# Kernel optimization log

Hardware: AMD Instinct MI355X
Metric: run time of the kernel (lower is better)

## Reference

```python
import jax, jax.numpy as jnp
import numpy as np


def setup_inputs() -> dict:
    key = jax.random.key(0)
    k1, k2, k3, k4, k5 = jax.random.split(key, 5)
    in_f, out_f, rank = 4096, 4096, 16
    std = 1.0 / np.sqrt(rank)
    x = jax.random.normal(k1, (4, 2048, in_f), dtype=jnp.float32)
    base_weight = jax.random.normal(k2, (out_f, in_f), dtype=jnp.float32) * 0.02
    lora_A = jax.random.normal(k3, (rank, in_f), dtype=jnp.float32) * std
    lora_B = jax.random.normal(k4, (out_f, rank), dtype=jnp.float32) * 0.01
    magnitude_vec = jax.random.uniform(k5, (out_f,), dtype=jnp.float32) + 0.5
    return {"x": x, "base_weight": base_weight, "lora_A": lora_A,
            "lora_B": lora_B, "magnitude_vec": magnitude_vec}


def reference(x, base_weight, lora_A, lora_B, magnitude_vec):
    # x: [B, S, in] -> tokens [N, in]
    out_shape = (*x.shape[:-1], base_weight.shape[0])
    xt = x.reshape(-1, x.shape[-1])
    # low-rank adapter path: [N, rank] @ [rank, out]
    lora_out = (xt @ lora_A.T) @ lora_B.T
    # column-wise L2 norm of adapted weight, per output row: [out]
    adapted_w = base_weight + lora_B @ lora_A
    column_norm = jnp.linalg.norm(adapted_w, axis=1)
    magnitude_scale = magnitude_vec / column_norm  # [out]
    # base GEMM + adapter + magnitude rescale epilogue
    dora_out = (xt @ base_weight.T + lora_out) * magnitude_scale[None, :]
    return dora_out.reshape(out_shape)
```

## Files before the change

kernel.cpp:

```cpp
#include <hip/hip_runtime.h>
#include <hip/hip_bf16.h>
#include <stdint.h>

typedef __attribute__((ext_vector_type(8))) short s16x8;
typedef __attribute__((ext_vector_type(4))) float f32x4;
typedef __attribute__((ext_vector_type(4))) unsigned short us4;

__device__ inline unsigned short bf_rne(float f) {
    union { float f; uint32_t u; } v; v.f = f;
    uint32_t u = v.u;
    u += 0x7FFFu + ((u >> 16) & 1u);
    return (unsigned short)(u >> 16);
}

#define GLD_LDS16(gp, lp)                                                     \
    __builtin_amdgcn_global_load_lds(                                         \
        (const __attribute__((address_space(1))) void*)(gp),                  \
        (__attribute__((address_space(3))) void*)(lp), 16, 0, 0)

#define LDSOFF(p) ((unsigned)(uintptr_t)(__attribute__((address_space(3))) const void*)(p))

__global__ __launch_bounds__(256) void prologue_kernel(
    const float4* __restrict__ x4, us4* __restrict__ xbf4,
    const float4* __restrict__ W4,
    const float4* __restrict__ A4,
    const float* __restrict__ B,
    const float* __restrict__ mag,
    unsigned short* __restrict__ wbf,
    float* __restrict__ scale) {
    const int tid = threadIdx.x;
    if (blockIdx.x < 512) {
        const int m0 = blockIdx.x * 8;
        __shared__ float Bs[8][16];
        __shared__ float red[32];
        if (tid < 128) Bs[tid >> 4][tid & 15] = B[m0 * 16 + tid];
        __syncthreads();
        float ss[8] = {};
        for (int c = tid; c < 1024; c += 256) {
            float4 a[16];
#pragma unroll
            for (int r = 0; r < 16; ++r) a[r] = A4[r * 1024 + c];
#pragma unroll
            for (int i = 0; i < 8; ++i) {
                float4 w = W4[(size_t)(m0 + i) * 1024 + c];
#pragma unroll
                for (int r = 0; r < 16; ++r) {
                    const float br = Bs[i][r];
                    w.x += br * a[r].x; w.y += br * a[r].y;
                    w.z += br * a[r].z; w.w += br * a[r].w;
                }
                ss[i] += w.x * w.x + w.y * w.y + w.z * w.z + w.w * w.w;
                us4 o; o[0] = bf_rne(w.x); o[1] = bf_rne(w.y);
                o[2] = bf_rne(w.z); o[3] = bf_rne(w.w);
                *(us4*)&wbf[(size_t)(m0 + i) * 4096 + c * 4] = o;
            }
        }
        const int lane = tid & 63, wv = tid >> 6;
#pragma unroll
        for (int i = 0; i < 8; ++i) {
            float v = ss[i];
#pragma unroll
            for (int off = 32; off > 0; off >>= 1) v += __shfl_down(v, off, 64);
            if (lane == 0) red[wv * 8 + i] = v;
        }
        __syncthreads();
        if (tid < 8) {
            float tot = red[tid] + red[8 + tid] + red[16 + tid] + red[24 + tid];
            scale[m0 + tid] = mag[m0 + tid] / sqrtf(tot);
        }
    } else {
        const size_t base = (size_t)(blockIdx.x - 512) * 1024 + tid;
#pragma unroll
        for (int j = 0; j < 4; ++j) {
            const size_t idx = base + j * 256;
            float4 a = x4[idx];
            us4 o;
            o[0] = bf_rne(a.x); o[1] = bf_rne(a.y);
            o[2] = bf_rne(a.z); o[3] = bf_rne(a.w);
            xbf4[idx] = o;
        }
    }
}

#define FENCE() asm volatile("" ::: "memory")
#define BAR()   do { FENCE(); __builtin_amdgcn_s_barrier(); FENCE(); } while (0)
#define VMW6()  asm volatile("s_waitcnt vmcnt(6)" ::: "memory")
#define VMW0()  asm volatile("s_waitcnt vmcnt(0)" ::: "memory")
#define LGW(n)  asm volatile("s_waitcnt lgkmcnt(" #n ")" ::: "memory")
#define SB0()   __builtin_amdgcn_sched_barrier(0)
#define PRIO1() __builtin_amdgcn_s_setprio(1)
#define PRIO0() __builtin_amdgcn_s_setprio(0)

#define DSR(dst, va, IMM) \
    asm volatile("ds_read_b128 %0, %1 offset:" #IMM : "=v"(dst) : "v"(va))

__global__ __launch_bounds__(512, 2) void dora_gemm(
    const unsigned short* __restrict__ xbf,
    const unsigned short* __restrict__ wbf,
    const float* __restrict__ scale,
    float* __restrict__ out) {
    __shared__ __align__(16) unsigned short As[2][256 * 64];
    __shared__ __align__(16) unsigned short Bs[2][256 * 64];

    const int tid  = threadIdx.x;
    const int lane = tid & 63;
    const int w    = tid >> 6;
    const int wm   = w >> 2;
    const int wn   = w & 3;
    const int q    = lane >> 4;
    const int c15  = lane & 15;

    const int bid = blockIdx.x;
    const int xcd = bid & 7, sub = bid >> 3;
    const int tileM = (((xcd & 3) << 3) | (sub & 7)) << 8;
    const int tileN = (((xcd >> 2) << 3) | (sub >> 3)) << 8;

    const int r0 = tid >> 3;
    const int lc = (tid & 7) ^ (r0 & 7);
    const size_t aoff = (size_t)(tileM + r0) * 4096 + lc * 8;
    const size_t boff = (size_t)(tileN + r0) * 4096 + lc * 8;
    const int ld0 = (w * 64) * 8;
    const int ld1 = (512 + w * 64) * 8;

#define STAGE_A(d, h, k0) do {                                                            \
    GLD_LDS16(xbf + aoff + (size_t)((h) * 128) * 4096 + (k0),      &As[d][(h) * 8192 + ld0]); \
    GLD_LDS16(xbf + aoff + (size_t)((h) * 128 + 64) * 4096 + (k0), &As[d][(h) * 8192 + ld1]); \
} while (0)
#define STAGE_B(d, h, k0) do {                                                            \
    GLD_LDS16(wbf + boff + (size_t)((h) * 128) * 4096 + (k0),      &Bs[d][(h) * 8192 + ld0]); \
    GLD_LDS16(wbf + boff + (size_t)((h) * 128 + 64) * 4096 + (k0), &Bs[d][(h) * 8192 + ld1]); \
} while (0)

    const int rb = c15 & 7;
    unsigned aA[4][2], aB[2][2];
#pragma unroll
    for (int mt = 0; mt < 4; ++mt)
#pragma unroll
        for (int kc = 0; kc < 2; ++kc)
            aA[mt][kc] = LDSOFF(&As[0][(wm * 64 + mt * 16 + c15) * 64 +
                                       ((kc * 4 + q) ^ rb) * 8]);
#pragma unroll
    for (int nt = 0; nt < 2; ++nt)
#pragma unroll
        for (int kc = 0; kc < 2; ++kc)
            aB[nt][kc] = LDSOFF(&Bs[0][(wn * 32 + nt * 16 + c15) * 64 +
                                       ((kc * 4 + q) ^ rb) * 8]);

    s16x8 af[4][2];
    s16x8 bfx[2][2][2];
    f32x4 acc[8][4] = {};

#define RD16(I0, I1) do {                                                     \
    DSR(bfx[0][0][0], aB[0][0], I0); DSR(bfx[0][1][0], aB[1][0], I0);         \
    DSR(af[0][0], aA[0][0], I0);     DSR(af[1][0], aA[1][0], I0);             \
    DSR(af[2][0], aA[2][0], I0);     DSR(af[3][0], aA[3][0], I0);             \
    DSR(bfx[0][0][1], aB[0][1], I0); DSR(bfx[0][1][1], aB[1][1], I0);         \
    DSR(af[0][1], aA[0][1], I0);     DSR(af[1][1], aA[1][1], I0);             \
    DSR(af[2][1], aA[2][1], I0);     DSR(af[3][1], aA[3][1], I0);             \
    DSR(bfx[1][0][0], aB[0][0], I1); DSR(bfx[1][1][0], aB[1][0], I1);         \
    DSR(bfx[1][0][1], aB[0][1], I1); DSR(bfx[1][1][1], aB[1][1], I1); } while (0)
#define RD_A1(IMM) do {                                                       \
    DSR(af[0][0], aA[0][0], IMM); DSR(af[1][0], aA[1][0], IMM);               \
    DSR(af[2][0], aA[2][0], IMM); DSR(af[3][0], aA[3][0], IMM);               \
    DSR(af[0][1], aA[0][1], IMM); DSR(af[1][1], aA[1][1], IMM);               \
    DSR(af[2][1], aA[2][1], IMM); DSR(af[3][1], aA[3][1], IMM); } while (0)

#define MFMA_H(mh, nh, kcv) do {                                              \
    _Pragma("unroll") for (int mt = 0; mt < 4; ++mt)                          \
    _Pragma("unroll") for (int nt = 0; nt < 2; ++nt)                          \
        acc[(mh) * 4 + mt][(nh) * 2 + nt] =                                   \
            __builtin_amdgcn_mfma_f32_16x16x32_bf16(                          \
                af[mt][kcv], bfx[nh][nt][kcv],                                \
                acc[(mh) * 4 + mt][(nh) * 2 + nt], 0, 0, 0);                  \
} while (0)
#define MFMA_Q(mh, nh) do { MFMA_H(mh, nh, 0); MFMA_H(mh, nh, 1); } while (0)

    STAGE_A(0, 0, 0); STAGE_B(0, 0, 0); STAGE_B(0, 1, 0); STAGE_A(0, 1, 0);
    STAGE_A(1, 0, 64); STAGE_B(1, 0, 64); STAGE_B(1, 1, 64);
    VMW6(); BAR();

    for (int t0k = 0; t0k <= 60 * 64; t0k += 128) {
        const int kt1 = t0k + 64;
        const int kn2 = t0k + 128;
        const int kn3 = t0k + 192;
        RD16(0, 16384);
        STAGE_A(1, 1, kt1);
        BAR();
        LGW(10); SB0(); PRIO1(); MFMA_H(0, 0, 0); PRIO0();
        LGW(4);  SB0(); PRIO1(); MFMA_H(0, 0, 1); PRIO0();
        BAR();
        LGW(0); SB0(); PRIO1(); MFMA_Q(0, 1); PRIO0();
        RD_A1(16384);
        STAGE_A(0, 0, kn2); STAGE_B(0, 0, kn2);
        BAR();
        LGW(4); SB0(); PRIO1(); MFMA_H(1, 1, 0); PRIO0();
        LGW(0); SB0(); PRIO1(); MFMA_H(1, 1, 1); PRIO0();
        STAGE_B(0, 1, kn2);
        VMW6(); BAR();
        PRIO1(); MFMA_Q(1, 0); PRIO0();
        RD16(32768, 49152);
        STAGE_A(0, 1, kn2);
        BAR();
        LGW(10); SB0(); PRIO1(); MFMA_H(0, 0, 0); PRIO0();
        LGW(4);  SB0(); PRIO1(); MFMA_H(0, 0, 1); PRIO0();
        BAR();
        LGW(0); SB0(); PRIO1(); MFMA_Q(0, 1); PRIO0();
        RD_A1(49152);
        STAGE_A(1, 0, kn3); STAGE_B(1, 0, kn3);
        BAR();
        LGW(4); SB0(); PRIO1(); MFMA_H(1, 1, 0); PRIO0();
        LGW(0); SB0(); PRIO1(); MFMA_H(1, 1, 1); PRIO0();
        STAGE_B(1, 1, kn3);
        VMW6(); BAR();
        PRIO1(); MFMA_Q(1, 0); PRIO0();
    }

    RD16(0, 16384);
    STAGE_A(1, 1, 4032);
    BAR();
    LGW(10); SB0(); PRIO1(); MFMA_H(0, 0, 0); PRIO0();
    LGW(4);  SB0(); PRIO1(); MFMA_H(0, 0, 1); PRIO0();
    BAR();
    LGW(0); SB0(); PRIO1(); MFMA_Q(0, 1); PRIO0();
    RD_A1(16384);
    BAR();
    LGW(4); SB0(); PRIO1(); MFMA_H(1, 1, 0); PRIO0();
    LGW(0); SB0(); PRIO1(); MFMA_H(1, 1, 1); PRIO0();
    VMW0(); BAR();
    PRIO1(); MFMA_Q(1, 0); PRIO0();
    RD16(32768, 49152);
    LGW(10); SB0(); PRIO1(); MFMA_H(0, 0, 0); PRIO0();
    LGW(4);  SB0(); PRIO1(); MFMA_H(0, 0, 1); PRIO0();
    LGW(0);  SB0(); PRIO1(); MFMA_Q(0, 1); PRIO0();
    RD_A1(49152);
    LGW(4); SB0(); PRIO1(); MFMA_H(1, 1, 0); PRIO0();
    LGW(0); SB0(); PRIO1(); MFMA_H(1, 1, 1); MFMA_Q(1, 0); PRIO0();

#pragma unroll
    for (int nh = 0; nh < 2; ++nh)
#pragma unroll
    for (int nt = 0; nt < 2; ++nt) {
        const int col = tileN + nh * 128 + wn * 32 + nt * 16 + c15;
        const float s = scale[col];
#pragma unroll
        for (int mh = 0; mh < 2; ++mh)
#pragma unroll
        for (int mt = 0; mt < 4; ++mt) {
            const int row0 = tileM + mh * 128 + wm * 64 + mt * 16 + q * 4;
#pragma unroll
            for (int r = 0; r < 4; ++r)
                out[(size_t)(row0 + r) * 4096 + col] = acc[mh * 4 + mt][nh * 2 + nt][r] * s;
        }
    }
}

extern "C" void kernel_launch(void* const* d_in, const int* in_sizes, int n_in,
                              void* d_out, int out_size, void* d_ws, size_t ws_size,
                              hipStream_t stream) {
    const float* x   = (const float*)d_in[0];
    const float* W   = (const float*)d_in[1];
    const float* A   = (const float*)d_in[2];
    const float* B   = (const float*)d_in[3];
    const float* mag = (const float*)d_in[4];
    float* out = (float*)d_out;

    const size_t XBF_BYTES = (size_t)8192 * 4096 * 2;
    const size_t WBF_BYTES = (size_t)4096 * 4096 * 2;
    const size_t NEEDED = XBF_BYTES + WBF_BYTES + 4096 * sizeof(float);
    if (ws_size < NEEDED) return;

    unsigned short* xbf = (unsigned short*)d_ws;
    unsigned short* wbf = (unsigned short*)((char*)d_ws + XBF_BYTES);
    float* scale = (float*)((char*)d_ws + XBF_BYTES + WBF_BYTES);

    prologue_kernel<<<8704, 256, 0, stream>>>((const float4*)x, (us4*)xbf,
                                              (const float4*)W, (const float4*)A,
                                              B, mag, wbf, scale);
    dora_gemm<<<512, 512, 0, stream>>>(xbf, wbf, scale, out);
}
```

Baseline: 307.2 us.

## Load B operand directly from global into registers, dropping LDS staging for weights

The weight (B) tile is no longer staged through shared memory. Each wave now issues buffer_load_dwordx4 straight into its MFMA operand registers, and only the activation tile goes through LDS. The main loop is rewritten into a simpler two-tile pipeline with fewer barriers. This halves LDS footprint and LDS read traffic, but B data is no longer shared across the waves in a block, so global/L2 traffic for weights grows and load latency must be hidden by the register prefetch.

```diff
diff --git a/kernel.cpp b/kernel.cpp
--- a/kernel.cpp
+++ b/kernel.cpp
@@ -5,6 +5,7 @@
 typedef __attribute__((ext_vector_type(8))) short s16x8;
 typedef __attribute__((ext_vector_type(4))) float f32x4;
 typedef __attribute__((ext_vector_type(4))) unsigned short us4;
+typedef __attribute__((ext_vector_type(4))) unsigned int u32x4;
 
 __device__ inline unsigned short bf_rne(float f) {
     union { float f; uint32_t u; } v; v.f = f;
@@ -84,8 +85,7 @@
 
 #define FENCE() asm volatile("" ::: "memory")
 #define BAR()   do { FENCE(); __builtin_amdgcn_s_barrier(); FENCE(); } while (0)
-#define VMW6()  asm volatile("s_waitcnt vmcnt(6)" ::: "memory")
-#define VMW0()  asm volatile("s_waitcnt vmcnt(0)" ::: "memory")
+#define VMW(n)  asm volatile("s_waitcnt vmcnt(" #n ")" ::: "memory")
 #define LGW(n)  asm volatile("s_waitcnt lgkmcnt(" #n ")" ::: "memory")
 #define SB0()   __builtin_amdgcn_sched_barrier(0)
 #define PRIO1() __builtin_amdgcn_s_setprio(1)
@@ -93,6 +93,10 @@
 
 #define DSR(dst, va, IMM) \
     asm volatile("ds_read_b128 %0, %1 offset:" #IMM : "=v"(dst) : "v"(va))
+
+#define BLD(dst, voff) \
+    asm volatile("buffer_load_dwordx4 %0, %1, %2, 0 offen" \
+                 : "=v"(dst) : "v"(voff), "s"(srd))
 
 __global__ __launch_bounds__(512, 2) void dora_gemm(
     const unsigned short* __restrict__ xbf,
@@ -100,7 +104,6 @@
     const float* __restrict__ scale,
     float* __restrict__ out) {
     __shared__ __align__(16) unsigned short As[2][256 * 64];
-    __shared__ __align__(16) unsigned short Bs[2][256 * 64];
 
     const int tid  = threadIdx.x;
     const int lane = tid & 63;
@@ -118,7 +121,6 @@
     const int r0 = tid >> 3;
     const int lc = (tid & 7) ^ (r0 & 7);
     const size_t aoff = (size_t)(tileM + r0) * 4096 + lc * 8;
-    const size_t boff = (size_t)(tileN + r0) * 4096 + lc * 8;
     const int ld0 = (w * 64) * 8;
     const int ld1 = (512 + w * 64) * 8;
 
@@ -126,44 +128,45 @@
     GLD_LDS16(xbf + aoff + (size_t)((h) * 128) * 4096 + (k0),      &As[d][(h) * 8192 + ld0]); \
     GLD_LDS16(xbf + aoff + (size_t)((h) * 128 + 64) * 4096 + (k0), &As[d][(h) * 8192 + ld1]); \
 } while (0)
-#define STAGE_B(d, h, k0) do {                                                            \
-    GLD_LDS16(wbf + boff + (size_t)((h) * 128) * 4096 + (k0),      &Bs[d][(h) * 8192 + ld0]); \
-    GLD_LDS16(wbf + boff + (size_t)((h) * 128 + 64) * 4096 + (k0), &Bs[d][(h) * 8192 + ld1]); \
-} while (0)
 
     const int rb = c15 & 7;
-    unsigned aA[4][2], aB[2][2];
+    unsigned aA[4][2];
 #pragma unroll
     for (int mt = 0; mt < 4; ++mt)
 #pragma unroll
         for (int kc = 0; kc < 2; ++kc)
             aA[mt][kc] = LDSOFF(&As[0][(wm * 64 + mt * 16 + c15) * 64 +
                                        ((kc * 4 + q) ^ rb) * 8]);
-#pragma unroll
-    for (int nt = 0; nt < 2; ++nt)
-#pragma unroll
-        for (int kc = 0; kc < 2; ++kc)
-            aB[nt][kc] = LDSOFF(&Bs[0][(wn * 32 + nt * 16 + c15) * 64 +
-                                       ((kc * 4 + q) ^ rb) * 8]);
+
+    const unsigned long long wb = (unsigned long long)(uintptr_t)wbf;
+    const u32x4 srd = { (unsigned)wb, (unsigned)(wb >> 32),
+                        0xFFFFFFFFu, 0x00020000u };
+    unsigned v000 = (unsigned)((tileN + wn * 32 + c15) * 8192 + q * 16);
+    unsigned v001 = v000 + 64;
+    unsigned v010 = v000 + 16 * 8192;
+    unsigned v011 = v010 + 64;
+    unsigned v100 = v000 + 128 * 8192;
+    unsigned v101 = v100 + 64;
+    unsigned v110 = v100 + 16 * 8192;
+    unsigned v111 = v110 + 64;
 
     s16x8 af[4][2];
     s16x8 bfx[2][2][2];
     f32x4 acc[8][4] = {};
 
-#define RD16(I0, I1) do {                                                     \
-    DSR(bfx[0][0][0], aB[0][0], I0); DSR(bfx[0][1][0], aB[1][0], I0);         \
-    DSR(af[0][0], aA[0][0], I0);     DSR(af[1][0], aA[1][0], I0);             \
-    DSR(af[2][0], aA[2][0], I0);     DSR(af[3][0], aA[3][0], I0);             \
-    DSR(bfx[0][0][1], aB[0][1], I0); DSR(bfx[0][1][1], aB[1][1], I0);         \
-    DSR(af[0][1], aA[0][1], I0);     DSR(af[1][1], aA[1][1], I0);             \
-    DSR(af[2][1], aA[2][1], I0);     DSR(af[3][1], aA[3][1], I0);             \
-    DSR(bfx[1][0][0], aB[0][0], I1); DSR(bfx[1][1][0], aB[1][0], I1);         \
-    DSR(bfx[1][0][1], aB[0][1], I1); DSR(bfx[1][1][1], aB[1][1], I1); } while (0)
-#define RD_A1(IMM) do {                                                       \
+#define BLD_B0() do { BLD(bfx[0][0][0], v000); BLD(bfx[0][0][1], v001);       \
+                      BLD(bfx[0][1][0], v010); BLD(bfx[0][1][1], v011); } while (0)
+#define BLD_B1() do { BLD(bfx[1][0][0], v100); BLD(bfx[1][0][1], v101);       \
+                      BLD(bfx[1][1][0], v110); BLD(bfx[1][1][1], v111); } while (0)
+#define VBUMP() do { v000 += 128; v001 += 128; v010 += 128; v011 += 128;      \
+                     v100 += 128; v101 += 128; v110 += 128; v111 += 128; } while (0)
+
+#define RD_A0(IMM) do {                                                       \
     DSR(af[0][0], aA[0][0], IMM); DSR(af[1][0], aA[1][0], IMM);               \
     DSR(af[2][0], aA[2][0], IMM); DSR(af[3][0], aA[3][0], IMM);               \
     DSR(af[0][1], aA[0][1], IMM); DSR(af[1][1], aA[1][1], IMM);               \
     DSR(af[2][1], aA[2][1], IMM); DSR(af[3][1], aA[3][1], IMM); } while (0)
+#define RD_A1(IMM) RD_A0(IMM)
 
 #define MFMA_H(mh, nh, kcv) do {                                              \
     _Pragma("unroll") for (int mt = 0; mt < 4; ++mt)                          \
@@ -173,68 +176,39 @@
                 af[mt][kcv], bfx[nh][nt][kcv],                                \
                 acc[(mh) * 4 + mt][(nh) * 2 + nt], 0, 0, 0);                  \
 } while (0)
-#define MFMA_Q(mh, nh) do { MFMA_H(mh, nh, 0); MFMA_H(mh, nh, 1); } while (0)
-
-    STAGE_A(0, 0, 0); STAGE_B(0, 0, 0); STAGE_B(0, 1, 0); STAGE_A(0, 1, 0);
-    STAGE_A(1, 0, 64); STAGE_B(1, 0, 64); STAGE_B(1, 1, 64);
-    VMW6(); BAR();
-
-    for (int t0k = 0; t0k <= 60 * 64; t0k += 128) {
-        const int kt1 = t0k + 64;
-        const int kn2 = t0k + 128;
-        const int kn3 = t0k + 192;
-        RD16(0, 16384);
-        STAGE_A(1, 1, kt1);
-        BAR();
-        LGW(10); SB0(); PRIO1(); MFMA_H(0, 0, 0); PRIO0();
-        LGW(4);  SB0(); PRIO1(); MFMA_H(0, 0, 1); PRIO0();
-        BAR();
-        LGW(0); SB0(); PRIO1(); MFMA_Q(0, 1); PRIO0();
-        RD_A1(16384);
-        STAGE_A(0, 0, kn2); STAGE_B(0, 0, kn2);
-        BAR();
-        LGW(4); SB0(); PRIO1(); MFMA_H(1, 1, 0); PRIO0();
-        LGW(0); SB0(); PRIO1(); MFMA_H(1, 1, 1); PRIO0();
-        STAGE_B(0, 1, kn2);
-        VMW6(); BAR();
-        PRIO1(); MFMA_Q(1, 0); PRIO0();
-        RD16(32768, 49152);
-        STAGE_A(0, 1, kn2);
-        BAR();
-        LGW(10); SB0(); PRIO1(); MFMA_H(0, 0, 0); PRIO0();
-        LGW(4);  SB0(); PRIO1(); MFMA_H(0, 0, 1); PRIO0();
-        BAR();
-        LGW(0); SB0(); PRIO1(); MFMA_Q(0, 1); PRIO0();
-        RD_A1(49152);
-        STAGE_A(1, 0, kn3); STAGE_B(1, 0, kn3);
-        BAR();
-        LGW(4); SB0(); PRIO1(); MFMA_H(1, 1, 0); PRIO0();
-        LGW(0); SB0(); PRIO1(); MFMA_H(1, 1, 1); PRIO0();
-        STAGE_B(1, 1, kn3);
-        VMW6(); BAR();
-        PRIO1(); MFMA_Q(1, 0); PRIO0();
+
+#define TILEB(I0, I1, DD, KN) do {                                            \
+    VMW(8); BAR();                                                            \
+    STAGE_A(DD, 0, KN); STAGE_A(DD, 1, KN);                                   \
+    RD_A0(I0);                                                                \
+    VMW(4);                                                                   \
+    LGW(4); SB0(); PRIO1(); MFMA_H(0, 0, 0); PRIO0();                         \
+    LGW(0); SB0(); PRIO1(); MFMA_H(0, 0, 1); MFMA_H(0, 1, 0);                 \
+                           MFMA_H(0, 1, 1); PRIO0();                          \
+    RD_A1(I1);                                                                \
+    LGW(4); SB0(); PRIO1(); MFMA_H(1, 0, 0); PRIO0();                         \
+    LGW(0); SB0(); PRIO1(); MFMA_H(1, 0, 1); PRIO0();                         \
+    BLD_B0();                                                                 \
+    PRIO1(); MFMA_H(1, 1, 0); MFMA_H(1, 1, 1); PRIO0();                       \
+    BLD_B1(); VBUMP();                                                        \
+} while (0)
+
+    STAGE_A(0, 0, 0); STAGE_A(0, 1, 0);
+    BLD_B0(); BLD_B1(); VBUMP();
+
+    for (int kn = 64; kn <= 3904; kn += 128) {
+        TILEB(0, 16384, 1, kn);
+        TILEB(32768, 49152, 0, kn + 64);
     }
-
-    RD16(0, 16384);
-    STAGE_A(1, 1, 4032);
-    BAR();
-    LGW(10); SB0(); PRIO1(); MFMA_H(0, 0, 0); PRIO0();
-    LGW(4);  SB0(); PRIO1(); MFMA_H(0, 0, 1); PRIO0();
-    BAR();
-    LGW(0); SB0(); PRIO1(); MFMA_Q(0, 1); PRIO0();
-    RD_A1(16384);
-    BAR();
-    LGW(4); SB0(); PRIO1(); MFMA_H(1, 1, 0); PRIO0();
-    LGW(0); SB0(); PRIO1(); MFMA_H(1, 1, 1); PRIO0();
-    VMW0(); BAR();
-    PRIO1(); MFMA_Q(1, 0); PRIO0();
-    RD16(32768, 49152);
-    LGW(10); SB0(); PRIO1(); MFMA_H(0, 0, 0); PRIO0();
-    LGW(4);  SB0(); PRIO1(); MFMA_H(0, 0, 1); PRIO0();
-    LGW(0);  SB0(); PRIO1(); MFMA_Q(0, 1); PRIO0();
+    TILEB(0, 16384, 1, 4032);
+    VMW(8); BAR();
+    RD_A0(32768);
+    VMW(0);
+    LGW(4); SB0(); PRIO1(); MFMA_H(0, 0, 0); PRIO0();
+    LGW(0); SB0(); PRIO1(); MFMA_H(0, 0, 1); MFMA_H(0, 1, 0); MFMA_H(0, 1, 1); PRIO0();
     RD_A1(49152);
-    LGW(4); SB0(); PRIO1(); MFMA_H(1, 1, 0); PRIO0();
-    LGW(0); SB0(); PRIO1(); MFMA_H(1, 1, 1); MFMA_Q(1, 0); PRIO0();
+    LGW(4); SB0(); PRIO1(); MFMA_H(1, 0, 0); PRIO0();
+    LGW(0); SB0(); PRIO1(); MFMA_H(1, 0, 1); MFMA_H(1, 1, 0); MFMA_H(1, 1, 1); PRIO0();
 
 #pragma unroll
     for (int nh = 0; nh < 2; ++nh)
@@ -276,5 +250,5 @@
     prologue_kernel<<<8704, 256, 0, stream>>>((const float4*)x, (us4*)xbf,
                                               (const float4*)W, (const float4*)A,
                                               B, mag, wbf, scale);
-    dora_gemm<<<512, 512, 0, stream>>>(xbf, wbf, scale, out);
-}
+    dora_gemm<<<2048 / 4, 512, 0, stream>>>(xbf, wbf, scale, out);
+}
```

Result: slower. 389.9 us (+26.9%).
